# Optimization experiments

Measured on AMD Instinct MI355X. Metric: run time of the kernel, lower is better.

Reference implementation:

```python
import jax, jax.numpy as jnp
import numpy as np

B, N, DEG, LOOKBACK, DIM, OUT = 256, 512, 16, 5, 64, 6
E = B * N * DEG            # 2,097,152 directed edges
NN = B * N                 # 131,072 nodes
K1 = int(np.ceil(0.8 * N))    # 410 nodes kept per graph after pool1
K2 = int(np.ceil(0.8 * K1))   # 328 nodes kept per graph after pool2


def setup_inputs():
    key = jax.random.key(0)
    ks = jax.random.split(key, 14)
    x = jax.random.normal(ks[0], (NN, LOOKBACK), jnp.float32)
    # per-graph random edges, then shift into the global node index space
    local = jax.random.randint(ks[1], (2, E), 0, N)
    offsets = jnp.repeat(jnp.arange(B, dtype=jnp.int32) * N, N * DEG)
    edge_index = local + offsets[None, :]

    def lin(k, fi, fo):
        return jax.random.normal(k, (fi, fo), jnp.float32) / np.sqrt(fi)

    return {
        "x": x,
        "edge_index": edge_index,
        "c1_Wl": lin(ks[2], LOOKBACK, DIM), "c1_bl": jnp.zeros((DIM,), jnp.float32),
        "c1_Wr": lin(ks[3], LOOKBACK, DIM),
        "pool1_w": jax.random.normal(ks[4], (DIM,), jnp.float32) / np.sqrt(DIM),
        "c2_Wl": lin(ks[5], DIM, DIM), "c2_bl": jnp.zeros((DIM,), jnp.float32),
        "c2_Wr": lin(ks[6], DIM, DIM),
        "pool2_w": jax.random.normal(ks[7], (DIM,), jnp.float32) / np.sqrt(DIM),
        "lin1_W": lin(ks[8], 2 * DIM, DIM), "lin1_b": jnp.zeros((DIM,), jnp.float32),
        "lin2_W": lin(ks[9], DIM, OUT), "lin2_b": jnp.zeros((OUT,), jnp.float32),
    }


def _sage(x, src, dst, valid, Wl, bl, Wr, n_nodes):
    # PyG SAGEConv: out = lin_l(mean_{j->i} x_j) + lin_r(x_i); empty nbhd -> 0
    msg = x[src] * valid[:, None]
    s = jax.ops.segment_sum(msg, dst, num_segments=n_nodes)
    deg = jax.ops.segment_sum(valid, dst, num_segments=n_nodes)
    mean = s / jnp.maximum(deg, 1.0)[:, None]
    return mean @ Wl + bl + x @ Wr


def _topk(x, w, nb, npg, k):
    # PyG TopKPooling: score = tanh(x.w/||w||), keep top-k per graph, scale kept rows
    score = jnp.tanh((x @ w) / jnp.linalg.norm(w))
    vals, idx = jax.lax.top_k(score.reshape(nb, npg), k)     # [nb, k]
    perm = (idx + (jnp.arange(nb) * npg)[:, None]).reshape(-1)
    return x[perm] * vals.reshape(-1, 1), perm


def _readout(x, nb, k):
    r = x.reshape(nb, k, -1)
    return jnp.concatenate([r.max(axis=1), r.mean(axis=1)], axis=1)  # [gmp | gap]


def reference(x, edge_index, c1_Wl, c1_bl, c1_Wr, pool1_w,
              c2_Wl, c2_bl, c2_Wr, pool2_w, lin1_W, lin1_b, lin2_W, lin2_b):
    src, dst = edge_index[0], edge_index[1]
    valid0 = jnp.ones((E,), jnp.float32)

    h = jax.nn.relu(_sage(x, src, dst, valid0, c1_Wl, c1_bl, c1_Wr, NN))
    h, perm1 = _topk(h, pool1_w, B, N, K1)
    x1 = _readout(h, B, K1)

    # filter_adj: remap edges to pooled node ids, mask dropped edges
    n1 = B * K1
    inv = jnp.full((NN,), -1, jnp.int32).at[perm1].set(jnp.arange(n1, dtype=jnp.int32))
    s1, d1 = inv[src], inv[dst]
    valid1 = ((s1 >= 0) & (d1 >= 0)).astype(jnp.float32)
    s1 = jnp.maximum(s1, 0)
    d1 = jnp.maximum(d1, 0)

    h = jax.nn.relu(_sage(h, s1, d1, valid1, c2_Wl, c2_bl, c2_Wr, n1))
    h, _ = _topk(h, pool2_w, B, K1, K2)
    x2 = _readout(h, B, K2)

    z = x1 + x2
    z = jax.nn.relu(z @ lin1_W + lin1_b)
    return z @ lin2_W + lin2_b
```

## Files before the change

### kernel.cpp

```cpp
#include <hip/hip_runtime.h>
#include <hip/hip_bf16.h>

#define BGR   256
#define NPG1  512
#define DEG   16
#define EPG   (NPG1 * DEG)
#define LB    5
#define DIM   64
#define OUTF  6
#define NN    (BGR * NPG1)
#define EDG   (BGR * EPG)
#define K1    410
#define K2    328
#define N1    (BGR * K1)
#define K1P   (K1 + 1)
#define NR    (BGR * K1P)
#define CSRW  48
#define CSRW1 56
#define GRIDW (NR / 64)
#define GRIDA (N1 / 16)

__global__ __launch_bounds__(512)
void s1_csr_score_kernel(const float* __restrict__ x,
                         const int* __restrict__ eidx,
                         const float* __restrict__ Wl,
                         const float* __restrict__ bl,
                         const float* __restrict__ Wr,
                         const float* __restrict__ pw,
                         float* __restrict__ meanv,
                         float* __restrict__ sc1g) {
    __shared__ __align__(16) float xl[NPG1 * LB];
    __shared__ unsigned short lcsr[CSRW1 * NPG1];
    __shared__ int lcnt[NPG1];

    const int g = blockIdx.x, t = threadIdx.x;
    const int* __restrict__ src = eidx;
    const int* __restrict__ dst = eidx + EDG;

    {
        const float4* x4 = (const float4*)(x + (size_t)g * (NPG1 * LB));
        float4* xl4 = (float4*)xl;
        #pragma unroll
        for (int k = 0; k < 2; ++k) {
            int i = k * 512 + t;
            if (i < NPG1 * LB / 4) xl4[i] = x4[i];
        }
        lcnt[t] = 0;
    }
    __syncthreads();

    const int ebase = g * EPG;
    for (int k = 0; k < EPG / 512; ++k) {
        int e = ebase + k * 512 + t;
        int s = src[e] & (NPG1 - 1);
        int d = dst[e] & (NPG1 - 1);
        int slot = atomicAdd(&lcnt[d], 1);
        if (slot < CSRW1) lcsr[slot * NPG1 + d] = (unsigned short)s;
    }
    __syncthreads();

    const int dgf = lcnt[t];
    const int dg  = min(dgf, CSRW1);
    float s0 = 0.f, s1 = 0.f, s2 = 0.f, s3 = 0.f, s4 = 0.f;
    for (int k = 0; k < dg; ++k) {
        int s = lcsr[k * NPG1 + t];
        const float* xp = xl + s * LB;
        s0 += xp[0]; s1 += xp[1]; s2 += xp[2]; s3 += xp[3]; s4 += xp[4];
    }
    const float invd = 1.f / fmaxf((float)dgf, 1.f);
    float m[LB]  = { s0 * invd, s1 * invd, s2 * invd, s3 * invd, s4 * invd };
    float xv[LB];
    const int n = g * NPG1 + t;
    #pragma unroll
    for (int j = 0; j < LB; ++j) { xv[j] = xl[t * LB + j]; meanv[(size_t)n * LB + j] = m[j]; }

    const float4* Wl4 = (const float4*)Wl;
    const float4* Wr4 = (const float4*)Wr;
    const float4* bl4 = (const float4*)bl;
    const float4* pw4 = (const float4*)pw;
    float p = 0.f, q = 0.f;
    #pragma unroll 4
    for (int d4 = 0; d4 < DIM / 4; ++d4) {
        float4 bb = bl4[d4];
        float4 ww = pw4[d4];
        float4 h = bb;
        #pragma unroll
        for (int j = 0; j < LB; ++j) {
            float4 a = Wl4[j * (DIM / 4) + d4];
            float4 b = Wr4[j * (DIM / 4) + d4];
            h.x += m[j] * a.x + xv[j] * b.x;
            h.y += m[j] * a.y + xv[j] * b.y;
            h.z += m[j] * a.z + xv[j] * b.z;
            h.w += m[j] * a.w + xv[j] * b.w;
        }
        h.x = fmaxf(h.x, 0.f); h.y = fmaxf(h.y, 0.f);
        h.z = fmaxf(h.z, 0.f); h.w = fmaxf(h.w, 0.f);
        p += h.x * ww.x + h.y * ww.y + h.z * ww.z + h.w * ww.w;
        q += ww.x * ww.x + ww.y * ww.y + ww.z * ww.z + ww.w * ww.w;
    }
    sc1g[n] = tanhf(p / sqrtf(q));
}

__global__ __launch_bounds__(512)
void s1_rankpool_kernel(const float* __restrict__ x,
                        const float* __restrict__ meanv,
                        const float* __restrict__ sc1g,
                        const float* __restrict__ Wl,
                        const float* __restrict__ bl,
                        const float* __restrict__ Wr,
                        float* __restrict__ h1p,
                        int* __restrict__ invr,
                        float* __restrict__ x1buf) {
    __shared__ __align__(16) float sc[NPG1];
    __shared__ int   rnk[NPG1];
    __shared__ float redmx[8 * DIM];
    __shared__ float redsm[8 * DIM];

    const int g = blockIdx.x, t = threadIdx.x;
    const int wid = t >> 6, lane = t & 63;

    sc[t] = sc1g[g * NPG1 + t];
    if (t < DIM) h1p[((size_t)g * K1P + K1) * DIM + t] = 0.f;
    __syncthreads();

    {
        float my = sc[t];
        int r = 0;
        const float4* sc4 = (const float4*)sc;
        #pragma unroll 4
        for (int j4 = 0; j4 < NPG1 / 4; ++j4) {
            float4 v = sc4[j4];
            int j = 4 * j4;
            r += (v.x > my) | ((v.x == my) & (j     < t));
            r += (v.y > my) | ((v.y == my) & (j + 1 < t));
            r += (v.z > my) | ((v.z == my) & (j + 2 < t));
            r += (v.w > my) | ((v.w == my) & (j + 3 < t));
        }
        rnk[t] = r;
        invr[g * NPG1 + t] = (r < K1) ? r : -1;
    }
    __syncthreads();

    float wlv[LB], wrv[LB];
    #pragma unroll
    for (int j = 0; j < LB; ++j) { wlv[j] = Wl[j * DIM + lane]; wrv[j] = Wr[j * DIM + lane]; }
    const float blv = bl[lane];

    float mx = -INFINITY, sm = 0.f;
    for (int n = wid; n < NPG1; n += 8) {
        int r = rnk[n];
        if (r >= K1) continue;
        const float* mp = meanv + (size_t)(g * NPG1 + n) * LB;
        const float* xp = x + (size_t)(g * NPG1 + n) * LB;
        float al = 0.f, ar = 0.f;
        #pragma unroll
        for (int j = 0; j < LB; ++j) {
            al += mp[j] * wlv[j];
            ar += xp[j] * wrv[j];
        }
        float acc = fmaxf(blv + al + ar, 0.f);
        float v = acc * sc[n];
        h1p[((size_t)g * K1P + r) * DIM + lane] = v;
        mx = fmaxf(mx, v);
        sm += v;
    }
    redmx[wid * DIM + lane] = mx;
    redsm[wid * DIM + lane] = sm;
    __syncthreads();
    if (wid == 0) {
        float m2 = redmx[lane], s2 = redsm[lane];
        #pragma unroll
        for (int w = 1; w < 8; ++w) {
            m2 = fmaxf(m2, redmx[w * DIM + lane]);
            s2 += redsm[w * DIM + lane];
        }
        x1buf[g * 2 * DIM + lane]       = m2;
        x1buf[g * 2 * DIM + DIM + lane] = s2 * (1.0f / (float)K1);
    }
}

__global__ __launch_bounds__(512)
void csr2_build_kernel(const int* __restrict__ eidx,
                       const int* __restrict__ invr,
                       unsigned short* __restrict__ csr2,
                       int* __restrict__ indeg) {
    __shared__ short linv[NPG1];
    __shared__ __align__(16) unsigned short lcsr[K1 * CSRW];
    __shared__ int lcnt[K1];

    const int g = blockIdx.x, t = threadIdx.x;
    const int* __restrict__ src = eidx;
    const int* __restrict__ dst = eidx + EDG;

    if (t < NPG1) linv[t] = (short)invr[g * NPG1 + t];
    if (t < K1) lcnt[t] = 0;
    {
        const int fill = (K1 << 16) | K1;
        int* li = (int*)lcsr;
        for (int i = t; i < K1 * CSRW / 2; i += 512) li[i] = fill;
    }
    __syncthreads();

    const int ebase = g * EPG;
    for (int k = 0; k < EPG / 512; ++k) {
        int e = ebase + k * 512 + t;
        int rs = linv[src[e] & (NPG1 - 1)];
        int rd = linv[dst[e] & (NPG1 - 1)];
        if ((rs | rd) >= 0) {
            int slot = atomicAdd(&lcnt[rd], 1);
            if (slot < CSRW) lcsr[rd * CSRW + slot] = (unsigned short)rs;
        }
    }
    __syncthreads();

    {
        const int4* ls4 = (const int4*)lcsr;
        int4* gs4 = (int4*)(csr2 + (size_t)g * K1 * CSRW);
        for (int i = t; i < K1 * CSRW / 8; i += 512) gs4[i] = ls4[i];
        if (t < K1) indeg[g * K1 + t] = min(lcnt[t], CSRW);
    }
}

__global__ __launch_bounds__(512)
void gemm2_kernel(float* __restrict__ hY,
                  float* __restrict__ Yr,
                  const float* __restrict__ Wl,
                  const float* __restrict__ bl,
                  const float* __restrict__ Wr) {
    __shared__ __align__(16) float wls[DIM * DIM];
    __shared__ __align__(16) float wrs[DIM * DIM];
    __shared__ __align__(16) float rt[64 * DIM];

    const int t = threadIdx.x, wid = t >> 6, lane = t & 63;
    const int nb = (int)blockIdx.x * 64;

    {
        const float4* W4l = (const float4*)Wl;
        const float4* W4r = (const float4*)Wr;
        const float4* R4  = (const float4*)&hY[(size_t)nb * DIM];
        float4* a = (float4*)wls;
        float4* b = (float4*)wrs;
        float4* r = (float4*)rt;
        #pragma unroll
        for (int k = 0; k < 2; ++k) {
            a[k * 512 + t] = W4l[k * 512 + t];
            b[k * 512 + t] = W4r[k * 512 + t];
            r[k * 512 + t] = R4[k * 512 + t];
        }
    }
    __syncthreads();

    const int r0 = wid * 8;
    float accl[8] = {0.f,0.f,0.f,0.f,0.f,0.f,0.f,0.f};
    float accr[8] = {0.f,0.f,0.f,0.f,0.f,0.f,0.f,0.f};
    #pragma unroll 4
    for (int j4 = 0; j4 < DIM / 4; ++j4) {
        const int jb = 4 * j4 * DIM + lane;
        float w0 = wls[jb],           w1 = wls[jb + DIM];
        float w2 = wls[jb + 2 * DIM], w3 = wls[jb + 3 * DIM];
        float u0 = wrs[jb],           u1 = wrs[jb + DIM];
        float u2 = wrs[jb + 2 * DIM], u3 = wrs[jb + 3 * DIM];
        #pragma unroll
        for (int i = 0; i < 8; ++i) {
            float4 a = *(const float4*)&rt[(r0 + i) * DIM + 4 * j4];
            accl[i] += a.x * w0 + a.y * w1 + a.z * w2 + a.w * w3;
            accr[i] += a.x * u0 + a.y * u1 + a.z * u2 + a.w * u3;
        }
    }
    const float bv = bl[lane];
    #pragma unroll
    for (int i = 0; i < 8; ++i) {
        hY[(size_t)(nb + r0 + i) * DIM + lane] = accl[i];
        Yr[(size_t)(nb + r0 + i) * DIM + lane] = accr[i] + bv;
    }
}

__global__ __launch_bounds__(256)
void gather2_kernel(const float* __restrict__ Yl,
                    float* __restrict__ Yh,
                    const unsigned short* __restrict__ csr2,
                    const int* __restrict__ indeg,
                    const float* __restrict__ pw,
                    float* __restrict__ sc2g) {
    const int t = threadIdx.x, wid = t >> 6, lane = t & 63;
    const int cid = ((int)blockIdx.x & 7) * (GRIDA / 8) + ((int)blockIdx.x >> 3);
    const int nb = __builtin_amdgcn_readfirstlane(cid * 16 + wid * 4);

    const float pwv = pw[lane];
    float q = pwv * pwv;
    #pragma unroll
    for (int o = 32; o; o >>= 1) q += __shfl_xor(q, o);
    const float inv_nrm = 1.f / sqrtf(q);

    #pragma unroll
    for (int i = 0; i < 4; ++i) {
        const int n  = nb + i;
        const int dg = indeg[n];
        const int g  = n / K1;
        const int lr = n - g * K1;
        const float* __restrict__ bp = Yl + (size_t)g * K1P * DIM;
        const int4* cr = (const int4*)(csr2 + (size_t)n * CSRW);
        float a0 = 0.f, a1 = 0.f;
        const int it = (dg + 7) >> 3;
        for (int kc = 0; kc < it; ++kc) {
            int4 wv = cr[kc];
            a0 += bp[((wv.x & 0xffff) << 6) + lane];
            a1 += bp[((wv.x >> 16)    << 6) + lane];
            a0 += bp[((wv.y & 0xffff) << 6) + lane];
            a1 += bp[((wv.y >> 16)    << 6) + lane];
            a0 += bp[((wv.z & 0xffff) << 6) + lane];
            a1 += bp[((wv.z >> 16)    << 6) + lane];
            a0 += bp[((wv.w & 0xffff) << 6) + lane];
            a1 += bp[((wv.w >> 16)    << 6) + lane];
        }
        const float invd = 1.f / fmaxf((float)dg, 1.f);
        float* yrow = Yh + (size_t)(g * K1P + lr) * DIM;
        const float h = fmaxf((a0 + a1) * invd + yrow[lane], 0.f);
        yrow[lane] = h;
        float p = h * pwv;
        #pragma unroll
        for (int o = 32; o; o >>= 1) p += __shfl_xor(p, o);
        if (lane == 0) sc2g[n] = tanhf(p * inv_nrm);
    }
}

__global__ __launch_bounds__(512)
void pool2_mlp_kernel(const float* __restrict__ sc2g,
                      const float* __restrict__ h2,
                      const float* __restrict__ x1buf,
                      const float* __restrict__ W1,
                      const float* __restrict__ b1,
                      const float* __restrict__ W2,
                      const float* __restrict__ b2,
                      float* __restrict__ out) {
    __shared__ __align__(16) float sc2[412];
    __shared__ int   rnk2[K1];
    __shared__ float redmx[8 * DIM];
    __shared__ float redsm[8 * DIM];
    __shared__ float zy[2 * DIM + DIM];

    const int g = blockIdx.x, t = threadIdx.x;
    const int wid = t >> 6, lane = t & 63;

    if (t < K1) sc2[t] = sc2g[g * K1 + t];
    if (t >= K1 && t < 412) sc2[t] = -INFINITY;
    __syncthreads();

    if (t < K1) {
        float my = sc2[t];
        int r = 0;
        const float4* sc4 = (const float4*)sc2;
        #pragma unroll 4
        for (int j4 = 0; j4 < 103; ++j4) {
            float4 v = sc4[j4];
            int j = 4 * j4;
            r += (v.x > my) | ((v.x == my) & (j     < t));
            r += (v.y > my) | ((v.y == my) & (j + 1 < t));
            r += (v.z > my) | ((v.z == my) & (j + 2 < t));
            r += (v.w > my) | ((v.w == my) & (j + 3 < t));
        }
        rnk2[t] = r;
    }
    __syncthreads();

    float mx = -INFINITY, sm = 0.f;
    for (int n = wid; n < K1; n += 8) {
        if (rnk2[n] < K2) {
            float v = h2[((size_t)g * K1P + n) * DIM + lane] * sc2[n];
            mx = fmaxf(mx, v);
            sm += v;
        }
    }
    redmx[wid * DIM + lane] = mx;
    redsm[wid * DIM + lane] = sm;
    __syncthreads();
    if (wid == 0) {
        float m2 = redmx[lane], s2 = redsm[lane];
        #pragma unroll
        for (int w = 1; w < 8; ++w) {
            m2 = fmaxf(m2, redmx[w * DIM + lane]);
            s2 += redsm[w * DIM + lane];
        }
        zy[lane]       = x1buf[g * 2 * DIM + lane]       + m2;
        zy[DIM + lane] = x1buf[g * 2 * DIM + DIM + lane] + s2 * (1.0f / (float)K2);
    }
    __syncthreads();

    if (t < DIM) {
        float a = b1[t];
        #pragma unroll 8
        for (int j = 0; j < 2 * DIM; ++j) a += zy[j] * W1[j * DIM + t];
        zy[2 * DIM + t] = fmaxf(a, 0.f);
    }
    __syncthreads();
    if (t < OUTF) {
        float a = b2[t];
        #pragma unroll
        for (int j = 0; j < DIM; ++j) a += zy[2 * DIM + j] * W2[j * OUTF + t];
        out[g * OUTF + t] = a;
    }
}

extern "C" void kernel_launch(void* const* d_in, const int* in_sizes, int n_in,
                              void* d_out, int out_size, void* d_ws, size_t ws_size,
                              hipStream_t stream) {
    (void)in_sizes; (void)n_in; (void)out_size; (void)ws_size;
    const float* x       = (const float*)d_in[0];
    const int*   eidx    = (const int*)d_in[1];
    const float* c1_Wl   = (const float*)d_in[2];
    const float* c1_bl   = (const float*)d_in[3];
    const float* c1_Wr   = (const float*)d_in[4];
    const float* pool1_w = (const float*)d_in[5];
    const float* c2_Wl   = (const float*)d_in[6];
    const float* c2_bl   = (const float*)d_in[7];
    const float* c2_Wr   = (const float*)d_in[8];
    const float* pool2_w = (const float*)d_in[9];
    const float* lin1_W  = (const float*)d_in[10];
    const float* lin1_b  = (const float*)d_in[11];
    const float* lin2_W  = (const float*)d_in[12];
    const float* lin2_b  = (const float*)d_in[13];
    float* out = (float*)d_out;

    char* w = (char*)d_ws;
    size_t off = 0;
    auto alloc = [&](size_t bytes) {
        void* p = w + off;
        off = (off + bytes + 255) & ~(size_t)255;
        return p;
    };
    float* h1p   = (float*)alloc((size_t)NR * DIM * 4);
    int*   invr  = (int*)  alloc((size_t)NN * 4);
    float* x1buf = (float*)alloc((size_t)BGR * 2 * DIM * 4);
    float* sc2g  = (float*)alloc((size_t)N1 * 4);
    int*   indeg = (int*)  alloc((size_t)N1 * 4);
    float* Yh    = (float*)alloc((size_t)NR * DIM * 4);
    char*  csreg = (char*) alloc((size_t)N1 * CSRW * 2);

    float* Yl    = h1p;
    unsigned short* csr2 = (unsigned short*)csreg;
    float* meanv = (float*)csreg;
    float* sc1g  = meanv + (size_t)NN * LB;

    s1_csr_score_kernel<<<BGR, 512, 0, stream>>>(x, eidx, c1_Wl, c1_bl, c1_Wr,
                                                 pool1_w, meanv, sc1g);
    s1_rankpool_kernel<<<BGR, 512, 0, stream>>>(x, meanv, sc1g, c1_Wl, c1_bl,
                                                c1_Wr, h1p, invr, x1buf);
    csr2_build_kernel<<<BGR, 512, 0, stream>>>(eidx, invr, csr2, indeg);
    gemm2_kernel<<<GRIDW, 512, 0, stream>>>(h1p, Yh, c2_Wl, c2_bl, c2_Wr);
    gather2_kernel<<<GRIDA, 256, 0, stream>>>(Yl, Yh, csr2, indeg, pool2_w, sc2g);
    pool2_mlp_kernel<<<BGR, 512, 0, stream>>>(sc2g, Yh, x1buf, lin1_W, lin1_b,
                                              lin2_W, lin2_b, out);
}
```

Baseline: 183.5 us.

## Restructure gemm2 to one row per lane with uniform weight loads

The layer-2 GEMM kernel no longer stages both 64x64 weight matrices in LDS. Each lane now holds one full input row in registers and computes 32 output columns. Each wave handles one half of either Wl or Wr, reading weights with wave-uniform addresses that can become scalar loads. The row tile is padded to stride 68 to avoid LDS bank conflicts, blocks shrink to 256 threads, and outputs are written as float4. This cuts LDS traffic and footprint for higher occupancy, at the cost of heavy register pressure (64 row values plus 32 accumulators).

```diff
diff --git a/kernel.cpp b/kernel.cpp
--- a/kernel.cpp
+++ b/kernel.cpp
@@ -17,6 +17,7 @@
 #define NR    (BGR * K1P)
 #define CSRW  48
 #define CSRW1 56
+#define RSTR  68
 #define GRIDW (NR / 64)
 #define GRIDA (N1 / 16)
 
@@ -221,57 +222,66 @@
     }
 }
 
-__global__ __launch_bounds__(512)
+__global__ __launch_bounds__(256)
 void gemm2_kernel(float* __restrict__ hY,
                   float* __restrict__ Yr,
                   const float* __restrict__ Wl,
                   const float* __restrict__ bl,
                   const float* __restrict__ Wr) {
-    __shared__ __align__(16) float wls[DIM * DIM];
-    __shared__ __align__(16) float wrs[DIM * DIM];
-    __shared__ __align__(16) float rt[64 * DIM];
-
-    const int t = threadIdx.x, wid = t >> 6, lane = t & 63;
+    __shared__ __align__(16) float rt[64 * RSTR];
+
+    const int t = threadIdx.x;
     const int nb = (int)blockIdx.x * 64;
 
     {
-        const float4* W4l = (const float4*)Wl;
-        const float4* W4r = (const float4*)Wr;
-        const float4* R4  = (const float4*)&hY[(size_t)nb * DIM];
-        float4* a = (float4*)wls;
-        float4* b = (float4*)wrs;
-        float4* r = (float4*)rt;
-        #pragma unroll
-        for (int k = 0; k < 2; ++k) {
-            a[k * 512 + t] = W4l[k * 512 + t];
-            b[k * 512 + t] = W4r[k * 512 + t];
-            r[k * 512 + t] = R4[k * 512 + t];
-        }
-    }
-    __syncthreads();
-
-    const int r0 = wid * 8;
-    float accl[8] = {0.f,0.f,0.f,0.f,0.f,0.f,0.f,0.f};
-    float accr[8] = {0.f,0.f,0.f,0.f,0.f,0.f,0.f,0.f};
-    #pragma unroll 4
-    for (int j4 = 0; j4 < DIM / 4; ++j4) {
-        const int jb = 4 * j4 * DIM + lane;
-        float w0 = wls[jb],           w1 = wls[jb + DIM];
-        float w2 = wls[jb + 2 * DIM], w3 = wls[jb + 3 * DIM];
-        float u0 = wrs[jb],           u1 = wrs[jb + DIM];
-        float u2 = wrs[jb + 2 * DIM], u3 = wrs[jb + 3 * DIM];
-        #pragma unroll
-        for (int i = 0; i < 8; ++i) {
-            float4 a = *(const float4*)&rt[(r0 + i) * DIM + 4 * j4];
-            accl[i] += a.x * w0 + a.y * w1 + a.z * w2 + a.w * w3;
-            accr[i] += a.x * u0 + a.y * u1 + a.z * u2 + a.w * u3;
-        }
-    }
-    const float bv = bl[lane];
-    #pragma unroll
-    for (int i = 0; i < 8; ++i) {
-        hY[(size_t)(nb + r0 + i) * DIM + lane] = accl[i];
-        Yr[(size_t)(nb + r0 + i) * DIM + lane] = accr[i] + bv;
+        const float4* G = (const float4*)&hY[(size_t)nb * DIM];
+        #pragma unroll
+        for (int k = 0; k < 4; ++k) {
+            int c = k * 256 + t;
+            int r = c >> 4, j4 = c & 15;
+            *(float4*)&rt[r * RSTR + 4 * j4] = G[c];
+        }
+    }
+    __syncthreads();
+
+    const int lane = t & 63;
+    const int wid  = __builtin_amdgcn_readfirstlane(t >> 6);
+    const int cb   = (wid & 1) << 5;
+    const bool isR = (wid & 2) != 0;
+    const float* __restrict__ wmat = isR ? Wr : Wl;
+    float* __restrict__ outp = isR ? Yr : hY;
+
+    float rv[DIM];
+    #pragma unroll
+    for (int k = 0; k < DIM / 4; ++k) {
+        float4 v = *(const float4*)&rt[lane * RSTR + 4 * k];
+        rv[4 * k] = v.x; rv[4 * k + 1] = v.y; rv[4 * k + 2] = v.z; rv[4 * k + 3] = v.w;
+    }
+
+    float acc[32];
+    #pragma unroll
+    for (int c = 0; c < 32; ++c) acc[c] = 0.f;
+
+    #pragma unroll
+    for (int j = 0; j < DIM; ++j) {
+        const float* __restrict__ wr_ = wmat + j * DIM + cb;
+        #pragma unroll
+        for (int c = 0; c < 32; ++c)
+            acc[c] += rv[j] * wr_[c];
+    }
+
+    if (isR) {
+        #pragma unroll
+        for (int c = 0; c < 32; ++c) acc[c] += bl[cb + c];
+    }
+
+    float* orow = outp + (size_t)(nb + lane) * DIM + cb;
+    #pragma unroll
+    for (int k = 0; k < 8; ++k) {
+        float4 v;
+        v.x = acc[4 * k]; v.y = acc[4 * k + 1];
+        v.z = acc[4 * k + 2]; v.w = acc[4 * k + 3];
+        *(float4*)&orow[4 * k] = v;
     }
 }
 
@@ -446,7 +456,7 @@
     s1_rankpool_kernel<<<BGR, 512, 0, stream>>>(x, meanv, sc1g, c1_Wl, c1_bl,
                                                 c1_Wr, h1p, invr, x1buf);
     csr2_build_kernel<<<BGR, 512, 0, stream>>>(eidx, invr, csr2, indeg);
-    gemm2_kernel<<<GRIDW, 512, 0, stream>>>(h1p, Yh, c2_Wl, c2_bl, c2_Wr);
+    gemm2_kernel<<<GRIDW, 256, 0, stream>>>(h1p, Yh, c2_Wl, c2_bl, c2_Wr);
     gather2_kernel<<<GRIDA, 256, 0, stream>>>(Yl, Yh, csr2, indeg, pool2_w, sc2g);
     pool2_mlp_kernel<<<BGR, 512, 0, stream>>>(sc2g, Yh, x1buf, lin1_W, lin1_b,
                                               lin2_W, lin2_b, out);
```

Measured after the change: 188.5 us. 1.03x slower.
